# Optimization experiments

Measured on AMD Instinct MI355X. Metric: run time of the kernel, lower is better.

The kernel has to match this reference:

```python
import math
import jax, jax.numpy as jnp
import numpy as np

H = 16  # n_heads


def setup_inputs() -> dict:
    key = jax.random.key(0)
    ks = jax.random.split(key, 12)
    b, n, dm = 4, 1024, 1024
    s = 1.0 / math.sqrt(dm)
    inp = {
        'query': jax.random.normal(ks[0], (b, n, dm), jnp.float32),
        'key':   jax.random.normal(ks[1], (b, n, dm), jnp.float32),
        'value': jax.random.normal(ks[2], (b, n, dm), jnp.float32),
        'Wq': jax.random.normal(ks[3], (dm, dm), jnp.float32) * s,
        'bq': jnp.zeros((dm,), jnp.float32),
        'Wk': jax.random.normal(ks[4], (dm, dm), jnp.float32) * s,
        'bk': jnp.zeros((dm,), jnp.float32),
        'Wv': jax.random.normal(ks[5], (dm, dm), jnp.float32) * s,
        'bv': jnp.zeros((dm,), jnp.float32),
        'Wo': jax.random.normal(ks[6], (dm, dm), jnp.float32) * s,
        'bo': jnp.zeros((dm,), jnp.float32),
    }
    return inp


def reference(query, key, value, Wq, bq, Wk, bk, Wv, bv, Wo, bo):
    b, n, dm = query.shape
    dk = dm // H

    def proj(x, W, bias):
        # Linear(d_model,d_model) then split heads: [b,n,dm] -> [b,h,n,dk]
        y = x @ W.T + bias
        return y.reshape(b, n, H, dk).transpose(0, 2, 1, 3)

    q = proj(query, Wq, bq)
    k = proj(key, Wk, bk)
    v = proj(value, Wv, bv)

    scores = jnp.einsum('bhid,bhjd->bhij', q, k) / math.sqrt(dk)  # [b,h,n,n]
    p_attn = jax.nn.softmax(scores, axis=-1)
    # softmax(ones) along last dim is exactly uniform 1/n
    p_ident = jnp.full_like(scores, 1.0 / n)
    rnd = jax.random.normal(jax.random.key(42), scores.shape, scores.dtype)
    p_rand = jax.nn.softmax(rnd, axis=-1)

    # FAITHFUL to source: einsum('b h i j, b h i d -> b h i d', p, value)
    # i.e. value scaled by row-sum of the attention probs (== value up to numerics)
    def weight(p):
        return v * jnp.sum(p, axis=-1, keepdims=True)  # [b,h,n,dk]

    x = weight(p_attn)
    y = weight(p_ident)
    z = weight(p_rand)

    def merge(t):  # [b,h,n,dk] -> [b,n,dm]
        return t.transpose(0, 2, 1, 3).reshape(b, n, dm)

    return (merge(x) @ Wo.T + bo, merge(y), merge(z))
```

## Files before the change

### kernel.cpp

```cpp
#include <hip/hip_runtime.h>
#include <hip/hip_bf16.h>
#include <stdint.h>

using bf16 = __hip_bfloat16;
typedef __attribute__((ext_vector_type(8))) __bf16 bf16x8;
typedef __attribute__((ext_vector_type(4))) float f32x4;

static __device__ __forceinline__ bf16 f2b(float x) { return __float2bfloat16(x); }
static __device__ __forceinline__ uint32_t pack2(float a, float b) {
    bf16 ha = f2b(a), hb = f2b(b);
    return (uint32_t)(*(const uint16_t*)&ha) | ((uint32_t)(*(const uint16_t*)&hb) << 16);
}

__global__ __launch_bounds__(256) void prep_w_kernel(
    const float* __restrict__ Wv,
    bf16* __restrict__ Wv_b, bf16* __restrict__ WvT_b, int dm)
{
    __shared__ bf16 tile[32][34];
    const int t = blockIdx.x;
    const int tid = threadIdx.x;
    const int tpr = dm / 32;
    const int i0 = (t / tpr) * 32, j0 = (t % tpr) * 32;
    const int tx = tid & 31, ty = tid >> 5;
    #pragma unroll
    for (int p = 0; p < 4; ++p) {
        const int r = ty + p * 8;
        const bf16 h = f2b(Wv[(size_t)(i0 + r) * dm + j0 + tx]);
        Wv_b[(size_t)(i0 + r) * dm + j0 + tx] = h;
        tile[r][tx] = h;
    }
    __syncthreads();
    #pragma unroll
    for (int p = 0; p < 4; ++p) {
        const int c = ty + p * 8;
        WvT_b[(size_t)(j0 + c) * dm + i0 + tx] = tile[tx][c];
    }
}

__global__ __launch_bounds__(256, 4) void mix_kernel(
    const bf16* __restrict__ B,
    const float* __restrict__ value, const float* __restrict__ Wo,
    const float* __restrict__ bv, const float* __restrict__ bo,
    bf16* __restrict__ Wc_b, bf16* __restrict__ value_b, float* __restrict__ bc,
    int nbWc, int nbVal, int dm)
{
    __shared__ bf16 As[64 * 64];
    __shared__ bf16 Bs[64 * 64];

    const int blk = blockIdx.x;
    const int tid = threadIdx.x;

    if (blk < nbWc) {
        const int K = dm, N = dm;
        const int tpr = dm / 64;
        const int bm = (blk / tpr) * 64, bn = (blk % tpr) * 64;
        const int lane = tid & 63;
        const int wave = tid >> 6;
        const int wm = (wave >> 1) * 32;
        const int wn = (wave & 1) * 32;

        f32x4 acc[2][2] = {};

        const int s0 = wave * 128 + lane;
        const int s1 = s0 + 64;
        const int r0 = s0 >> 3, r1 = s1 >> 3;
        const int p0 = (s0 & 7) ^ (r0 & 7);
        const int p1 = (s1 & 7) ^ (r1 & 7);
        const bf16* gB0 = B + (size_t)(bn + r0) * K + p0 * 8;
        const bf16* gB1 = B + (size_t)(bn + r1) * K + p1 * 8;
        bf16* lB0 = Bs + s0 * 8;
        bf16* lB1 = Bs + s1 * 8;

        const int sa0 = tid, sa1 = tid + 256;
        const int ra0 = sa0 >> 3, pa0 = (sa0 & 7) ^ (ra0 & 7);
        const int ra1 = sa1 >> 3, pa1 = (sa1 & 7) ^ (ra1 & 7);
        const float* gA0 = Wo + (size_t)(bm + ra0) * K + pa0 * 8;
        const float* gA1 = Wo + (size_t)(bm + ra1) * K + pa1 * 8;

        const int fr = lane & 15;
        const int fkc = lane >> 4;
        const int xb = fr & 7;

        for (int k0 = 0; k0 < K; k0 += 64) {
            __builtin_amdgcn_global_load_lds(
                (const __attribute__((address_space(1))) void*)(gB0 + k0),
                (__attribute__((address_space(3))) void*)lB0, 16, 0, 0);
            __builtin_amdgcn_global_load_lds(
                (const __attribute__((address_space(1))) void*)(gB1 + k0),
                (__attribute__((address_space(3))) void*)lB1, 16, 0, 0);
            const float4 a0 = *(const float4*)(gA0 + k0);
            const float4 a1 = *(const float4*)(gA0 + k0 + 4);
            const float4 a2 = *(const float4*)(gA1 + k0);
            const float4 a3 = *(const float4*)(gA1 + k0 + 4);
            uint4 u0 = { pack2(a0.x, a0.y), pack2(a0.z, a0.w),
                         pack2(a1.x, a1.y), pack2(a1.z, a1.w) };
            uint4 u1 = { pack2(a2.x, a2.y), pack2(a2.z, a2.w),
                         pack2(a3.x, a3.y), pack2(a3.z, a3.w) };
            *(uint4*)(As + sa0 * 8) = u0;
            *(uint4*)(As + sa1 * 8) = u1;
            __syncthreads();

            #pragma unroll
            for (int kk = 0; kk < 2; ++kk) {
                const int xsw = ((kk * 4 + fkc) ^ xb) * 8;
                bf16x8 af[2], bg[2];
                #pragma unroll
                for (int u = 0; u < 2; ++u) {
                    af[u] = *(const bf16x8*)(As + (wm + u * 16 + fr) * 64 + xsw);
                    bg[u] = *(const bf16x8*)(Bs + (wn + u * 16 + fr) * 64 + xsw);
                }
                #pragma unroll
                for (int i = 0; i < 2; ++i)
                    #pragma unroll
                    for (int j = 0; j < 2; ++j)
                        acc[i][j] = __builtin_amdgcn_mfma_f32_16x16x32_bf16(
                            af[i], bg[j], acc[i][j], 0, 0, 0);
            }
            __syncthreads();
        }

        const int quad = lane >> 4;
        #pragma unroll
        for (int j = 0; j < 2; ++j) {
            const int col = bn + wn + j * 16 + fr;
            #pragma unroll
            for (int i = 0; i < 2; ++i) {
                const int row0 = bm + wm + i * 16 + quad * 4;
                #pragma unroll
                for (int r = 0; r < 4; ++r)
                    Wc_b[(size_t)(row0 + r) * N + col] = f2b(acc[i][j][r]);
            }
        }
    } else if (blk < nbWc + nbVal) {
        const size_t i = ((size_t)(blk - nbWc) * 256 + tid) * 8;
        const float4 v0 = *(const float4*)(value + i);
        const float4 v1 = *(const float4*)(value + i + 4);
        uint4 u = { pack2(v0.x, v0.y), pack2(v0.z, v0.w),
                    pack2(v1.x, v1.y), pack2(v1.z, v1.w) };
        *(uint4*)(value_b + i) = u;
    } else {
        const int lane = tid & 63;
        const int wave = tid >> 6;
        const int row = (blk - nbWc - nbVal) * 4 + wave;
        const float* wrow = Wo + (size_t)row * dm;
        float s = 0.f;
        for (int k = lane * 4; k < dm; k += 256) {
            const float4 w = *(const float4*)(wrow + k);
            const float4 x = *(const float4*)(bv + k);
            s += w.x * x.x + w.y * x.y + w.z * x.z + w.w * x.w;
        }
        #pragma unroll
        for (int off = 32; off >= 1; off >>= 1) s += __shfl_down(s, off, 64);
        if (lane == 0) bc[row] = s + bo[row];
    }
}

#define TM 128
#define TN 128
#define BK 64

__global__ __launch_bounds__(256, 2) void gemm_fused(
    const bf16* __restrict__ A, const bf16* __restrict__ Bcat,
    const float* __restrict__ bv, const float* __restrict__ bc,
    float* __restrict__ out0, float* __restrict__ out1, float* __restrict__ out2,
    int M, int dm)
{
    __shared__ bf16 As[TM * BK];
    __shared__ bf16 Bs[TN * BK];
    __shared__ float Es[4][16 * 68];

    const int K = dm;
    const int tid = threadIdx.x;
    const int lane = tid & 63;
    const int wave = tid >> 6;
    const int wm = (wave >> 1) * 64;
    const int wn = (wave & 1) * 64;
    const int bm = blockIdx.x * TM;
    const int bn = blockIdx.y * TN;

    f32x4 acc[4][4] = {};

    const bf16* gA[4]; const bf16* gB[4];
    bf16* lA[4]; bf16* lB[4];
    #pragma unroll
    for (int q = 0; q < 4; ++q) {
        const int s = wave * 256 + q * 64 + lane;
        const int r = s >> 3;
        const int p = (s & 7) ^ (r & 7);
        gA[q] = A + (size_t)(bm + r) * K + p * 8;
        gB[q] = Bcat + (size_t)(bn + r) * K + p * 8;
        lA[q] = As + s * 8;
        lB[q] = Bs + s * 8;
    }

    const int fr = lane & 15;
    const int fkc = lane >> 4;
    const int xb = fr & 7;

    for (int k0 = 0; k0 < K; k0 += BK) {
        #pragma unroll
        for (int q = 0; q < 4; ++q)
            __builtin_amdgcn_global_load_lds(
                (const __attribute__((address_space(1))) void*)(gA[q] + k0),
                (__attribute__((address_space(3))) void*)lA[q], 16, 0, 0);
        #pragma unroll
        for (int q = 0; q < 4; ++q)
            __builtin_amdgcn_global_load_lds(
                (const __attribute__((address_space(1))) void*)(gB[q] + k0),
                (__attribute__((address_space(3))) void*)lB[q], 16, 0, 0);
        __syncthreads();

        #pragma unroll
        for (int kk = 0; kk < 2; ++kk) {
            const int xsw = ((kk * 4 + fkc) ^ xb) * 8;
            bf16x8 af[4], bg[4];
            #pragma unroll
            for (int t = 0; t < 4; ++t) {
                af[t] = *(const bf16x8*)(As + (wm + t * 16 + fr) * BK + xsw);
                bg[t] = *(const bf16x8*)(Bs + (wn + t * 16 + fr) * BK + xsw);
            }
            #pragma unroll
            for (int i = 0; i < 4; ++i)
                #pragma unroll
                for (int j = 0; j < 4; ++j)
                    acc[i][j] = __builtin_amdgcn_mfma_f32_16x16x32_bf16(
                        af[i], bg[j], acc[i][j], 0, 0, 0);
        }
        __syncthreads();
    }

    const bool second = (bn >= dm);
    const int colbase = bn + wn - (second ? dm : 0);
    const float* bias = second ? bc : bv;
    float* o0 = second ? out0 : out1;
    float* o1 = second ? nullptr : out2;

    float bb[4];
    #pragma unroll
    for (int j = 0; j < 4; ++j) bb[j] = bias[colbase + j * 16 + fr];

    float* E = &Es[wave][0];
    const int quad = lane >> 4;
    const int cc = (lane & 15) * 4;

    #pragma unroll
    for (int i = 0; i < 4; ++i) {
        #pragma unroll
        for (int j = 0; j < 4; ++j)
            #pragma unroll
            for (int r = 0; r < 4; ++r)
                E[(quad * 4 + r) * 68 + j * 16 + fr] = acc[i][j][r] + bb[j];
        #pragma unroll
        for (int ph = 0; ph < 4; ++ph) {
            const int row = quad * 4 + ph;
            const float4 v = *(const float4*)(E + row * 68 + cc);
            const size_t gi = (size_t)(bm + wm + i * 16 + row) * dm + colbase + cc;
            *(float4*)(o0 + gi) = v;
            if (o1) *(float4*)(o1 + gi) = v;
        }
    }
}

__global__ __launch_bounds__(256) void gemm_f32_naive(
    const float* __restrict__ A, const float* __restrict__ B,
    const float* __restrict__ bias,
    float* __restrict__ C0, float* __restrict__ C1,
    int M, int N, int K)
{
    const size_t idx = (size_t)blockIdx.x * 256 + threadIdx.x;
    if (idx >= (size_t)M * N) return;
    const int row = (int)(idx / N), col = (int)(idx % N);
    const float* a = A + (size_t)row * K;
    const float* b = B + (size_t)col * K;
    float s = bias ? bias[col] : 0.0f;
    for (int k = 0; k < K; ++k) s += a[k] * b[k];
    C0[idx] = s;
    if (C1) C1[idx] = s;
}

extern "C" void kernel_launch(void* const* d_in, const int* in_sizes, int n_in,
                              void* d_out, int out_size, void* d_ws, size_t ws_size,
                              hipStream_t stream)
{
    const float* value = (const float*)d_in[2];
    const float* Wv    = (const float*)d_in[7];
    const float* bv    = (const float*)d_in[8];
    const float* Wo    = (const float*)d_in[9];
    const float* bo    = (const float*)d_in[10];

    const int dm = in_sizes[8];
    const int M  = in_sizes[2] / dm;
    const size_t MN = (size_t)M * dm;

    float* out0 = (float*)d_out;
    float* out1 = out0 + MN;
    float* out2 = out1 + MN;

    const size_t dm2 = (size_t)dm * dm;
    const size_t need = MN * 2 + dm2 * 2 * 3 + (size_t)dm * 4;
    const bool ok = (ws_size >= need) && (M % TM == 0) && (dm % TM == 0) &&
                    (MN % 2048 == 0) && (dm2 % 2048 == 0) &&
                    (dm % 64 == 0) && (dm % 4 == 0);
    if (ok) {
        char* ws = (char*)d_ws;
        bf16* value_b = (bf16*)ws;   ws += MN * 2;
        bf16* Wv_b    = (bf16*)ws;   ws += dm2 * 2;
        bf16* Wc_b    = (bf16*)ws;   ws += dm2 * 2;
        bf16* WvT_b   = (bf16*)ws;   ws += dm2 * 2;
        float* bc     = (float*)ws;

        const int nbT = (dm / 32) * (dm / 32);
        prep_w_kernel<<<nbT, 256, 0, stream>>>(Wv, Wv_b, WvT_b, dm);

        const int nbWc  = (dm / 64) * (dm / 64);
        const int nbVal = (int)(MN / 2048);
        const int nbBc  = dm / 4;
        mix_kernel<<<nbWc + nbVal + nbBc, 256, 0, stream>>>(
            WvT_b, value, Wo, bv, bo, Wc_b, value_b, bc,
            nbWc, nbVal, dm);

        dim3 grid(M / TM, 2 * dm / TN);
        gemm_fused<<<grid, 256, 0, stream>>>(value_b, Wv_b, bv, bc,
                                             out0, out1, out2, M, dm);
    } else {
        const int nblk = (int)((MN + 255) / 256);
        gemm_f32_naive<<<nblk, 256, 0, stream>>>(value, Wv, bv, out1, out2, M, dm, dm);
        gemm_f32_naive<<<nblk, 256, 0, stream>>>(out1, Wo, bo, out0, nullptr, M, dm, dm);
    }
}
```

Measured before the change: 150.9 us.

## Fuse Wv transpose/convert into mix kernel and use nontemporal output stores

After: 157.2 us. 4.1% more time.

```diff
diff --git a/kernel.cpp b/kernel.cpp
--- a/kernel.cpp
+++ b/kernel.cpp
@@ -12,40 +12,17 @@
     return (uint32_t)(*(const uint16_t*)&ha) | ((uint32_t)(*(const uint16_t*)&hb) << 16);
 }
 
-__global__ __launch_bounds__(256) void prep_w_kernel(
-    const float* __restrict__ Wv,
-    bf16* __restrict__ Wv_b, bf16* __restrict__ WvT_b, int dm)
-{
-    __shared__ bf16 tile[32][34];
-    const int t = blockIdx.x;
-    const int tid = threadIdx.x;
-    const int tpr = dm / 32;
-    const int i0 = (t / tpr) * 32, j0 = (t % tpr) * 32;
-    const int tx = tid & 31, ty = tid >> 5;
-    #pragma unroll
-    for (int p = 0; p < 4; ++p) {
-        const int r = ty + p * 8;
-        const bf16 h = f2b(Wv[(size_t)(i0 + r) * dm + j0 + tx]);
-        Wv_b[(size_t)(i0 + r) * dm + j0 + tx] = h;
-        tile[r][tx] = h;
-    }
-    __syncthreads();
-    #pragma unroll
-    for (int p = 0; p < 4; ++p) {
-        const int c = ty + p * 8;
-        WvT_b[(size_t)(j0 + c) * dm + i0 + tx] = tile[tx][c];
-    }
-}
-
-__global__ __launch_bounds__(256, 4) void mix_kernel(
-    const bf16* __restrict__ B,
-    const float* __restrict__ value, const float* __restrict__ Wo,
-    const float* __restrict__ bv, const float* __restrict__ bo,
-    bf16* __restrict__ Wc_b, bf16* __restrict__ value_b, float* __restrict__ bc,
-    int nbWc, int nbVal, int dm)
+__global__ __launch_bounds__(256, 4) void prep_mix_kernel(
+    const float* __restrict__ value, const float* __restrict__ Wv,
+    const float* __restrict__ Wo, const float* __restrict__ bv,
+    const float* __restrict__ bo,
+    bf16* __restrict__ value_b, bf16* __restrict__ Wv_b,
+    bf16* __restrict__ Wc_b, float* __restrict__ bc,
+    int nbWc, int nbWv, int nbVal, int dm)
 {
     __shared__ bf16 As[64 * 64];
     __shared__ bf16 Bs[64 * 64];
+    __shared__ bf16 Ts[64 * 68];
 
     const int blk = blockIdx.x;
     const int tid = threadIdx.x;
@@ -61,33 +38,19 @@
 
         f32x4 acc[2][2] = {};
 
-        const int s0 = wave * 128 + lane;
-        const int s1 = s0 + 64;
-        const int r0 = s0 >> 3, r1 = s1 >> 3;
-        const int p0 = (s0 & 7) ^ (r0 & 7);
-        const int p1 = (s1 & 7) ^ (r1 & 7);
-        const bf16* gB0 = B + (size_t)(bn + r0) * K + p0 * 8;
-        const bf16* gB1 = B + (size_t)(bn + r1) * K + p1 * 8;
-        bf16* lB0 = Bs + s0 * 8;
-        bf16* lB1 = Bs + s1 * 8;
-
         const int sa0 = tid, sa1 = tid + 256;
         const int ra0 = sa0 >> 3, pa0 = (sa0 & 7) ^ (ra0 & 7);
         const int ra1 = sa1 >> 3, pa1 = (sa1 & 7) ^ (ra1 & 7);
         const float* gA0 = Wo + (size_t)(bm + ra0) * K + pa0 * 8;
         const float* gA1 = Wo + (size_t)(bm + ra1) * K + pa1 * 8;
 
+        const int tx = tid & 15, ty = tid >> 4;
+
         const int fr = lane & 15;
         const int fkc = lane >> 4;
         const int xb = fr & 7;
 
         for (int k0 = 0; k0 < K; k0 += 64) {
-            __builtin_amdgcn_global_load_lds(
-                (const __attribute__((address_space(1))) void*)(gB0 + k0),
-                (__attribute__((address_space(3))) void*)lB0, 16, 0, 0);
-            __builtin_amdgcn_global_load_lds(
-                (const __attribute__((address_space(1))) void*)(gB1 + k0),
-                (__attribute__((address_space(3))) void*)lB1, 16, 0, 0);
             const float4 a0 = *(const float4*)(gA0 + k0);
             const float4 a1 = *(const float4*)(gA0 + k0 + 4);
             const float4 a2 = *(const float4*)(gA1 + k0);
@@ -98,6 +61,30 @@
                          pack2(a3.x, a3.y), pack2(a3.z, a3.w) };
             *(uint4*)(As + sa0 * 8) = u0;
             *(uint4*)(As + sa1 * 8) = u1;
+
+            #pragma unroll
+            for (int p = 0; p < 4; ++p) {
+                const int r = ty + p * 16;
+                const float4 w = *(const float4*)(Wv + (size_t)(k0 + r) * dm + bn + tx * 4);
+                uint2 t2;
+                t2.x = pack2(w.x, w.y);
+                t2.y = pack2(w.z, w.w);
+                *(uint2*)((uint16_t*)Ts + r * 68 + tx * 4) = t2;
+            }
+            __syncthreads();
+
+            #pragma unroll
+            for (int m = 0; m < 2; ++m) {
+                const int s = 2 * tid + m;
+                const int j = s >> 3, kb = s & 7;
+                const uint16_t* tp = (const uint16_t*)Ts + kb * 8 * 68 + j;
+                uint4 u;
+                u.x = (uint32_t)tp[0]      | ((uint32_t)tp[68]     << 16);
+                u.y = (uint32_t)tp[2 * 68] | ((uint32_t)tp[3 * 68] << 16);
+                u.z = (uint32_t)tp[4 * 68] | ((uint32_t)tp[5 * 68] << 16);
+                u.w = (uint32_t)tp[6 * 68] | ((uint32_t)tp[7 * 68] << 16);
+                *(uint4*)(Bs + j * 64 + ((kb ^ (j & 7)) * 8)) = u;
+            }
             __syncthreads();
 
             #pragma unroll
@@ -131,8 +118,15 @@
                     Wc_b[(size_t)(row0 + r) * N + col] = f2b(acc[i][j][r]);
             }
         }
-    } else if (blk < nbWc + nbVal) {
+    } else if (blk < nbWc + nbWv) {
         const size_t i = ((size_t)(blk - nbWc) * 256 + tid) * 8;
+        const float4 v0 = *(const float4*)(Wv + i);
+        const float4 v1 = *(const float4*)(Wv + i + 4);
+        uint4 u = { pack2(v0.x, v0.y), pack2(v0.z, v0.w),
+                    pack2(v1.x, v1.y), pack2(v1.z, v1.w) };
+        *(uint4*)(Wv_b + i) = u;
+    } else if (blk < nbWc + nbWv + nbVal) {
+        const size_t i = ((size_t)(blk - nbWc - nbWv) * 256 + tid) * 8;
         const float4 v0 = *(const float4*)(value + i);
         const float4 v1 = *(const float4*)(value + i + 4);
         uint4 u = { pack2(v0.x, v0.y), pack2(v0.z, v0.w),
@@ -141,7 +135,7 @@
     } else {
         const int lane = tid & 63;
         const int wave = tid >> 6;
-        const int row = (blk - nbWc - nbVal) * 4 + wave;
+        const int row = (blk - nbWc - nbWv - nbVal) * 4 + wave;
         const float* wrow = Wo + (size_t)row * dm;
         float s = 0.f;
         for (int k = lane * 4; k < dm; k += 256) {
@@ -165,9 +159,9 @@
     float* __restrict__ out0, float* __restrict__ out1, float* __restrict__ out2,
     int M, int dm)
 {
-    __shared__ bf16 As[TM * BK];
-    __shared__ bf16 Bs[TN * BK];
-    __shared__ float Es[4][16 * 68];
+    __shared__ __align__(16) char smem[(TM + TN) * BK * 2];
+    bf16* const As = (bf16*)smem;
+    bf16* const Bs = (bf16*)smem + TM * BK;
 
     const int K = dm;
     const int tid = threadIdx.x;
@@ -239,7 +233,7 @@
     #pragma unroll
     for (int j = 0; j < 4; ++j) bb[j] = bias[colbase + j * 16 + fr];
 
-    float* E = &Es[wave][0];
+    float* E = (float*)smem + wave * (16 * 68);
     const int quad = lane >> 4;
     const int cc = (lane & 15) * 4;
 
@@ -253,10 +247,10 @@
         #pragma unroll
         for (int ph = 0; ph < 4; ++ph) {
             const int row = quad * 4 + ph;
-            const float4 v = *(const float4*)(E + row * 68 + cc);
+            const f32x4 v = *(const f32x4*)(E + row * 68 + cc);
             const size_t gi = (size_t)(bm + wm + i * 16 + row) * dm + colbase + cc;
-            *(float4*)(o0 + gi) = v;
-            if (o1) *(float4*)(o1 + gi) = v;
+            __builtin_nontemporal_store(v, (f32x4*)(o0 + gi));
+            if (o1) __builtin_nontemporal_store(v, (f32x4*)(o1 + gi));
         }
     }
 }
@@ -297,27 +291,23 @@
     float* out2 = out1 + MN;
 
     const size_t dm2 = (size_t)dm * dm;
-    const size_t need = MN * 2 + dm2 * 2 * 3 + (size_t)dm * 4;
+    const size_t need = MN * 2 + dm2 * 2 * 2 + (size_t)dm * 4;
     const bool ok = (ws_size >= need) && (M % TM == 0) && (dm % TM == 0) &&
-                    (MN % 2048 == 0) && (dm2 % 2048 == 0) &&
-                    (dm % 64 == 0) && (dm % 4 == 0);
+                    (MN % 2048 == 0) && (dm2 % 2048 == 0) && (dm % 64 == 0);
     if (ok) {
         char* ws = (char*)d_ws;
         bf16* value_b = (bf16*)ws;   ws += MN * 2;
         bf16* Wv_b    = (bf16*)ws;   ws += dm2 * 2;
         bf16* Wc_b    = (bf16*)ws;   ws += dm2 * 2;
-        bf16* WvT_b   = (bf16*)ws;   ws += dm2 * 2;
         float* bc     = (float*)ws;
 
-        const int nbT = (dm / 32) * (dm / 32);
-        prep_w_kernel<<<nbT, 256, 0, stream>>>(Wv, Wv_b, WvT_b, dm);
-
         const int nbWc  = (dm / 64) * (dm / 64);
+        const int nbWv  = (int)(dm2 / 2048);
         const int nbVal = (int)(MN / 2048);
         const int nbBc  = dm / 4;
-        mix_kernel<<<nbWc + nbVal + nbBc, 256, 0, stream>>>(
-            WvT_b, value, Wo, bv, bo, Wc_b, value_b, bc,
-            nbWc, nbVal, dm);
+        prep_mix_kernel<<<nbWc + nbWv + nbVal + nbBc, 256, 0, stream>>>(
+            value, Wv, Wo, bv, bo, value_b, Wv_b, Wc_b, bc,
+            nbWc, nbWv, nbVal, dm);
 
         dim3 grid(M / TM, 2 * dm / TN);
         gemm_fused<<<grid, 256, 0, stream>>>(value_b, Wv_b, bv, bc,
```
